# Kernel optimization log

Hardware: AMD Instinct MI355X
Metric: run time of the kernel (lower is better)

The kernel has to match this reference:

```python
import jax, jax.numpy as jnp
import numpy as np

N = 50000
E = 800000
IN_C = 128
HID = 32
HEADS = 4
G = 512      # number of graphs in batch
OUT_C = 100
NEG_SLOPE = 0.2
EPS = 1e-16


def _gat_params(key, f_in, heads, c):
    k1, k2, k3, k4 = jax.random.split(key, 4)
    s = 1.0 / np.sqrt(f_in)
    return {
        'W': jax.random.uniform(k1, (heads * c, f_in), jnp.float32, -s, s),
        'att_src': jax.random.normal(k2, (heads, c), jnp.float32) * 0.1,
        'att_dst': jax.random.normal(k3, (heads, c), jnp.float32) * 0.1,
        'b': jnp.zeros((heads * c,), jnp.float32),
    }


def setup_inputs() -> dict:
    key = jax.random.key(0)
    ks = jax.random.split(key, 8)
    x = jax.random.normal(ks[0], (N, IN_C), jnp.float32)
    edge_index = jax.random.randint(ks[1], (2, E), 0, N, jnp.int64)
    batch = jnp.sort(jax.random.randint(ks[2], (N,), 0, G, jnp.int64))
    p1 = _gat_params(ks[3], IN_C, HEADS, HID)
    p2 = _gat_params(ks[4], HEADS * HID, HEADS, HID)
    p3 = _gat_params(ks[5], HEADS * HID, HEADS, HID)
    s = 1.0 / np.sqrt(HEADS * HID)
    fc_W = jax.random.uniform(ks[6], (OUT_C, HEADS * HID), jnp.float32, -s, s)
    fc_b = jnp.zeros((OUT_C,), jnp.float32)
    return {
        'x': x, 'edge_index': edge_index, 'batch': batch,
        'W1': p1['W'], 'as1': p1['att_src'], 'ad1': p1['att_dst'], 'b1': p1['b'],
        'W2': p2['W'], 'as2': p2['att_src'], 'ad2': p2['att_dst'], 'b2': p2['b'],
        'W3': p3['W'], 'as3': p3['att_src'], 'ad3': p3['att_dst'], 'b3': p3['b'],
        'fc_W': fc_W, 'fc_b': fc_b,
    }


def gat_conv(x, src, dst, W, att_src, att_dst, b):
    # x: [N, F_in] -> h: [N, H, C]
    h = (x @ W.T).reshape(N, HEADS, HID)
    a_src = jnp.einsum('nhc,hc->nh', h, att_src)   # [N, H]
    a_dst = jnp.einsum('nhc,hc->nh', h, att_dst)
    alpha = a_src[src] + a_dst[dst]                 # [E', H]
    alpha = jax.nn.leaky_relu(alpha, NEG_SLOPE)
    # segment softmax over incoming edges of each dst node
    m = jax.ops.segment_max(alpha, dst, num_segments=N)
    alpha = jnp.exp(alpha - m[dst])
    denom = jax.ops.segment_sum(alpha, dst, num_segments=N)
    alpha = alpha / (denom[dst] + EPS)
    msg = alpha[:, :, None] * h[src]                # [E', H, C]
    out = jax.ops.segment_sum(msg, dst, num_segments=N)
    return out.reshape(N, HEADS * HID) + b


def reference(x, edge_index, batch,
              W1, as1, ad1, b1, W2, as2, ad2, b2, W3, as3, ad3, b3,
              fc_W, fc_b):
    # add self loops (PyG GATConv default)
    loops = jnp.arange(N, dtype=edge_index.dtype)
    src = jnp.concatenate([edge_index[0], loops])
    dst = jnp.concatenate([edge_index[1], loops])
    h = jax.nn.elu(gat_conv(x, src, dst, W1, as1, ad1, b1))
    h = jax.nn.elu(gat_conv(h, src, dst, W2, as2, ad2, b2))
    h = jax.nn.elu(gat_conv(h, src, dst, W3, as3, ad3, b3))
    # global mean pool over graphs
    sums = jax.ops.segment_sum(h, batch, num_segments=G)        # [G, H*C]
    cnts = jax.ops.segment_sum(jnp.ones((N,), h.dtype), batch, num_segments=G)
    pooled = sums / jnp.maximum(cnts, 1.0)[:, None]
    # dropout p=0.5 is identity in eval mode
    return pooled @ fc_W.T + fc_b
```

## Files before the change

kernel.cpp:

```cpp
#include <hip/hip_runtime.h>
#include <math.h>

#define NN 50000
#define EE 800000
#define GG 512
#define OUTC 100
#define NEG 0.2f
#define STRIDE 64
#define NPART 8
#define PRNG (NN / NPART)
#define PCHUNK 4096
#define NCHUNK 196
#define SCAT_BLOCKS (NPART * NCHUNK)

#define WROWS 145
#define WCHUNKS 73
#define WLAYER (WCHUNKS * 512)

typedef unsigned int u32;
#define GLOBAL_AS __attribute__((address_space(1)))
#define LDS_AS __attribute__((address_space(3)))

typedef __attribute__((ext_vector_type(8))) short bf16x8;
typedef __attribute__((ext_vector_type(8))) short s16x8;
typedef __attribute__((ext_vector_type(8))) unsigned short us8;
typedef __attribute__((ext_vector_type(4))) float f32x4;

__device__ inline ushort f2bf(float v) {
  unsigned u = __float_as_uint(v);
  unsigned r = (u + 0x7fff + ((u >> 16) & 1)) >> 16;
  return (ushort)r;
}

__global__ __launch_bounds__(256) void k_scatter_prep(const int* __restrict__ ei,
    int* __restrict__ cursor, ushort* __restrict__ srcs,
    const float* __restrict__ W0, const float* __restrict__ W1, const float* __restrict__ W2,
    const float* __restrict__ as0, const float* __restrict__ as1, const float* __restrict__ as2,
    const float* __restrict__ ad0, const float* __restrict__ ad1, const float* __restrict__ ad2,
    ushort* __restrict__ wg) {
  if (blockIdx.x < SCAT_BLOCKS) {
    int part = blockIdx.x & (NPART - 1);
    int chunk = blockIdx.x >> 3;
    int plo = part * PRNG, phi = plo + PRNG;
    int base = chunk * PCHUNK + (threadIdx.x << 2);
    int4 d[4];
    bool lv[4];
#pragma unroll
    for (int it = 0; it < 4; ++it) {
      int e = base + (it << 10);
      lv[it] = (e < EE);
      if (lv[it]) d[it] = *(const int4*)&ei[EE + e];
      else        d[it] = make_int4(-1, -1, -1, -1);
    }
#pragma unroll
    for (int it = 0; it < 4; ++it) {
      if (!lv[it]) continue;
      int e = base + (it << 10);
      int4 dd = d[it];
      bool m0 = (dd.x >= plo) & (dd.x < phi);
      bool m1 = (dd.y >= plo) & (dd.y < phi);
      bool m2 = (dd.z >= plo) & (dd.z < phi);
      bool m3 = (dd.w >= plo) & (dd.w < phi);
      if (m0 | m1 | m2 | m3) {
        int4 s4 = *(const int4*)&ei[e];
        if (m0) { int p = atomicAdd(&cursor[dd.x], 1); if (p < STRIDE) srcs[(dd.x << 6) + p] = (ushort)s4.x; }
        if (m1) { int p = atomicAdd(&cursor[dd.y], 1); if (p < STRIDE) srcs[(dd.y << 6) + p] = (ushort)s4.y; }
        if (m2) { int p = atomicAdd(&cursor[dd.z], 1); if (p < STRIDE) srcs[(dd.z << 6) + p] = (ushort)s4.z; }
        if (m3) { int p = atomicAdd(&cursor[dd.w], 1); if (p < STRIDE) srcs[(dd.w << 6) + p] = (ushort)s4.w; }
      }
    }
  } else {
    int pb = blockIdx.x - SCAT_BLOCKS;
    int layer = pb / 68, bx = pb % 68;
    const float* W  = (layer == 0) ? W0 : (layer == 1) ? W1 : W2;
    const float* av = (layer == 0) ? as0 : (layer == 1) ? as1 : as2;
    const float* dv = (layer == 0) ? ad0 : (layer == 1) ? ad1 : ad2;
    ushort* wgL = wg + (size_t)layer * WLAYER;
    int idx = bx * 256 + threadIdx.x;
    if (bx < 64) {
      int row = idx >> 7, col = idx & 127;
      int c = col >> 3, j = col & 7;
      float v = W[idx];
      ushort hb = f2bf(v);
      float hf = __uint_as_float(((unsigned)hb) << 16);
      wgL[((size_t)c * WROWS + row) * 8 + j] = hb;
      wgL[((size_t)(16 + c) * WROWS + row) * 8 + j] = f2bf(v - hf);
    } else {
      int j2 = idx - 64 * 256;
      int j = j2 >> 7, k = j2 & 127;
      int head = j & 3;
      const float* vec = (j < 4) ? &av[head * 32] : &dv[head * 32];
      float dot = 0.f;
#pragma unroll
      for (int c = 0; c < 32; c++) dot += W[(head * 32 + c) * 128 + k] * vec[c];
      ushort hb = f2bf(dot);
      float hf = __uint_as_float(((unsigned)hb) << 16);
      int c16 = k >> 3, jj = k & 7;
      wgL[((size_t)c16 * WROWS + 128 + j) * 8 + jj] = hb;
      wgL[((size_t)(16 + c16) * WROWS + 128 + j) * 8 + jj] = f2bf(dot - hf);
      wgL[((size_t)c16 * WROWS + 136 + j) * 8 + jj] = 0;
      wgL[((size_t)(16 + c16) * WROWS + 136 + j) * 8 + jj] = 0;
    }
  }
}

__global__ __launch_bounds__(512) void k_gemm_mfma(const float* __restrict__ feat,
    const ushort* __restrict__ wg,
    short* __restrict__ hq, float* __restrict__ asp, float* __restrict__ adstf) {
  __shared__ alignas(16) ushort lds[WLAYER];
  int t = threadIdx.x;
  int wave = t >> 6, lane = t & 63;
  int quad = lane >> 4, r16 = lane & 15;

#pragma unroll
  for (int i = 0; i < 10; ++i) {
    int chunk = i * 8 + wave;
    if (chunk < WCHUNKS) {
      int off = chunk * 512 + lane * 8;
      __builtin_amdgcn_global_load_lds((const GLOBAL_AS u32*)&wg[off],
                                       (LDS_AS u32*)&lds[off], 16, 0, 0);
    }
  }

  int n0 = blockIdx.x * 128;
  int rowA = n0 + wave * 16 + r16;
  bool valid = rowA < NN;
  float4 f[8];
#pragma unroll
  for (int ks = 0; ks < 4; ++ks) {
    if (valid) {
      const float4* fp = (const float4*)&feat[(size_t)rowA * 128 + ks * 32 + quad * 8];
      f[ks * 2] = fp[0];
      f[ks * 2 + 1] = fp[1];
    } else {
      f[ks * 2] = make_float4(0.f, 0.f, 0.f, 0.f);
      f[ks * 2 + 1] = f[ks * 2];
    }
  }
  __syncthreads();

  f32x4 acc[9];
#pragma unroll
  for (int nt = 0; nt < 9; nt++) acc[nt] = (f32x4)0.f;

#pragma unroll
  for (int ks = 0; ks < 4; ks++) {
    bf16x8 ah, al;
    {
      float4 va = f[ks * 2], vb = f[ks * 2 + 1];
      float vv[8] = {va.x, va.y, va.z, va.w, vb.x, vb.y, vb.z, vb.w};
      us8 hh, ll;
#pragma unroll
      for (int j = 0; j < 8; j++) {
        ushort hb = f2bf(vv[j]);
        float hf = __uint_as_float(((unsigned)hb) << 16);
        hh[j] = hb;
        ll[j] = (ushort)(__float_as_uint(vv[j] - hf) >> 16);
      }
      ah = (bf16x8)hh;
      al = (bf16x8)ll;
    }
    int cc = ks * 4 + quad;
#pragma unroll
    for (int nt = 0; nt < 9; nt++) {
      int wrow = (nt < 8) ? (nt * 16 + r16) : (128 + r16);
      bf16x8 bh = *(const bf16x8*)&lds[((size_t)cc * WROWS + wrow) * 8];
      bf16x8 bl = *(const bf16x8*)&lds[((size_t)(16 + cc) * WROWS + wrow) * 8];
      acc[nt] = __builtin_amdgcn_mfma_f32_16x16x32_bf16(ah, bh, acc[nt], 0, 0, 0);
      acc[nt] = __builtin_amdgcn_mfma_f32_16x16x32_bf16(al, bh, acc[nt], 0, 0, 0);
      acc[nt] = __builtin_amdgcn_mfma_f32_16x16x32_bf16(ah, bl, acc[nt], 0, 0, 0);
    }
  }

#pragma unroll
  for (int reg = 0; reg < 4; reg++) {
    float am = 0.f;
#pragma unroll
    for (int nt = 0; nt < 8; nt++) am = fmaxf(am, fabsf(acc[nt][reg]));
#pragma unroll
    for (int off = 1; off < 16; off <<= 1) am = fmaxf(am, __shfl_xor(am, off));
    int node = n0 + wave * 16 + quad * 4 + reg;
    if (node < NN) {
      float amc = fmaxf(am, 1e-20f);
      float rq = 32767.f / amc;
      if (r16 < 4) asp[node * 8 + r16] = acc[8][reg];
      else if (r16 < 8) adstf[node * 4 + r16 - 4] = acc[8][reg];
      else if (r16 == 8) asp[node * 8 + 4] = amc * (1.f / 32767.f);
      short* dq = &hq[(size_t)node * 128 + r16];
#pragma unroll
      for (int nt = 0; nt < 8; nt++)
        dq[nt * 16] = (short)__float2int_rn(acc[nt][reg] * rq);
    }
  }
}

__global__ __launch_bounds__(256) void k_gather(const short* __restrict__ hq,
    const float* __restrict__ asp,
    const float4* __restrict__ adst,
    const int* __restrict__ cursor, const ushort* __restrict__ srcs,
    const float* __restrict__ bias, float* __restrict__ outf) {
  __shared__ alignas(16) int   s_src[2][4][4][16];
  __shared__ alignas(16) float s_wt[2][4][4][4][20];

  int wave = threadIdx.x >> 6, lane = threadIdx.x & 63;
  int grp = lane >> 4;
  int gl = lane & 15;
  int node = blockIdx.x * 16 + wave * 4 + grp;
  int head = gl >> 2;
  int c0 = gl << 3;

  int deg = 0, e0 = 0;
  float4 ad = make_float4(0.f, 0.f, 0.f, 0.f);
  if (node < NN) {
    deg = min(cursor[node], STRIDE);
    e0 = node << 6;
    ad = adst[node];
  }
  int rounds = (deg + 15) >> 4;

  float acc[8];
#pragma unroll
  for (int i = 0; i < 8; i++) acc[i] = 0.f;
  float ws0 = 0.f, ws1 = 0.f, ws2 = 0.f, ws3 = 0.f;
  float wself = 0.f;

  int nsn = 0, nlive = 0;

  auto phase1 = [&](int r) {
    int j = (r << 4) + gl;
    nlive = (j < deg);
    nsn = nlive ? (int)srcs[e0 + j] : 0;
  };

  auto phase2 = [&](int b) {
    float q0 = 0.f, q1 = 0.f, q2 = 0.f, q3 = 0.f;
    if (nlive) {
      const float4 a = *(const float4*)&asp[nsn * 8];
      float sc = asp[nsn * 8 + 4];
      float v, w0, w1, w2, w3;
      v = a.x + ad.x; v = v > 0.f ? v : NEG * v; w0 = __expf(v);
      v = a.y + ad.y; v = v > 0.f ? v : NEG * v; w1 = __expf(v);
      v = a.z + ad.z; v = v > 0.f ? v : NEG * v; w2 = __expf(v);
      v = a.w + ad.w; v = v > 0.f ? v : NEG * v; w3 = __expf(v);
      ws0 += w0; ws1 += w1; ws2 += w2; ws3 += w3;
      q0 = w0 * sc; q1 = w1 * sc; q2 = w2 * sc; q3 = w3 * sc;
    }
    s_src[b][wave][grp][gl] = nsn << 7;
    s_wt[b][wave][grp][0][gl] = q0;
    s_wt[b][wave][grp][1][gl] = q1;
    s_wt[b][wave][grp][2][gl] = q2;
    s_wt[b][wave][grp][3][gl] = q3;
  };

  auto consume = [&](int r, int b) {
    int cnt = deg - (r << 4);
    cnt = min(cnt, 16);
    const int* srow = &s_src[b][wave][grp][0];
    const float* wrow = &s_wt[b][wave][grp][head][0];
#pragma unroll
    for (int c = 0; c < 2; ++c) {
      int k0 = c << 3;
      if (k0 < cnt) {
        int4 sa = *(const int4*)&srow[k0];
        int4 sb = *(const int4*)&srow[k0 + 4];
        float4 wa = *(const float4*)&wrow[k0];
        float4 wb = *(const float4*)&wrow[k0 + 4];
        s16x8 qa = *(const s16x8*)&hq[sa.x + c0];
        s16x8 qb = *(const s16x8*)&hq[sa.y + c0];
        s16x8 qc = *(const s16x8*)&hq[sa.z + c0];
        s16x8 qd = *(const s16x8*)&hq[sa.w + c0];
        s16x8 qe = *(const s16x8*)&hq[sb.x + c0];
        s16x8 qf = *(const s16x8*)&hq[sb.y + c0];
        s16x8 qg = *(const s16x8*)&hq[sb.z + c0];
        s16x8 qh = *(const s16x8*)&hq[sb.w + c0];
#pragma unroll
        for (int i = 0; i < 8; i++) acc[i] = fmaf(wa.x, (float)qa[i], acc[i]);
#pragma unroll
        for (int i = 0; i < 8; i++) acc[i] = fmaf(wa.y, (float)qb[i], acc[i]);
#pragma unroll
        for (int i = 0; i < 8; i++) acc[i] = fmaf(wa.z, (float)qc[i], acc[i]);
#pragma unroll
        for (int i = 0; i < 8; i++) acc[i] = fmaf(wa.w, (float)qd[i], acc[i]);
        if (k0 + 4 < cnt) {
#pragma unroll
          for (int i = 0; i < 8; i++) acc[i] = fmaf(wb.x, (float)qe[i], acc[i]);
#pragma unroll
          for (int i = 0; i < 8; i++) acc[i] = fmaf(wb.y, (float)qf[i], acc[i]);
#pragma unroll
          for (int i = 0; i < 8; i++) acc[i] = fmaf(wb.z, (float)qg[i], acc[i]);
#pragma unroll
          for (int i = 0; i < 8; i++) acc[i] = fmaf(wb.w, (float)qh[i], acc[i]);
        }
      }
    }
  };

  phase1(0);

  if (node < NN) {
    const float4 a = *(const float4*)&asp[node * 8];
    float sc = asp[node * 8 + 4];
    float v, w0, w1, w2, w3;
    v = a.x + ad.x; v = v > 0.f ? v : NEG * v; w0 = __expf(v);
    v = a.y + ad.y; v = v > 0.f ? v : NEG * v; w1 = __expf(v);
    v = a.z + ad.z; v = v > 0.f ? v : NEG * v; w2 = __expf(v);
    v = a.w + ad.w; v = v > 0.f ? v : NEG * v; w3 = __expf(v);
    float wh = (head == 0) ? w0 : (head == 1) ? w1 : (head == 2) ? w2 : w3;
    wself = wh;
    float wssc = wh * sc;
    s16x8 qs = *(const s16x8*)&hq[(node << 7) + c0];
#pragma unroll
    for (int i = 0; i < 8; i++) acc[i] = wssc * (float)qs[i];
  }

  if (rounds > 0) {
    phase2(0);
    for (int r = 0; r < rounds; ++r) {
      int b = r & 1;
      if (r + 1 < rounds) phase1(r + 1);
      consume(r, b);
      if (r + 1 < rounds) phase2(b ^ 1);
    }
  }

#pragma unroll
  for (int off = 1; off < 16; off <<= 1) {
    ws0 += __shfl_xor(ws0, off);
    ws1 += __shfl_xor(ws1, off);
    ws2 += __shfl_xor(ws2, off);
    ws3 += __shfl_xor(ws3, off);
  }

  if (node < NN) {
    float wsum = wself + ((head == 0) ? ws0 : (head == 1) ? ws1 : (head == 2) ? ws2 : ws3);
    float rcp = 1.f / (wsum + 1e-16f);
    float4 bv0 = *(const float4*)&bias[c0];
    float4 bv1 = *(const float4*)&bias[c0 + 4];
    float bb[8] = {bv0.x, bv0.y, bv0.z, bv0.w, bv1.x, bv1.y, bv1.z, bv1.w};
    float o[8];
#pragma unroll
    for (int i = 0; i < 8; i++) {
      float v = acc[i] * rcp + bb[i];
      o[i] = v > 0.f ? v : expm1f(v);
    }
    *(float4*)&outf[(size_t)node * 128 + c0] = make_float4(o[0], o[1], o[2], o[3]);
    *(float4*)&outf[(size_t)node * 128 + c0 + 4] = make_float4(o[4], o[5], o[6], o[7]);
  }
}

__global__ __launch_bounds__(128) void k_pool(const float* __restrict__ feat,
    const int* __restrict__ batch, float* __restrict__ pooled, float* __restrict__ cnt) {
  int n0 = blockIdx.x * 32;
  int c = threadIdx.x;
  float acc = 0.f; int curg = -1;
  for (int i = 0; i < 32; i++) {
    int n = n0 + i;
    if (n >= NN) break;
    int g = batch[n];
    if (g != curg) {
      if (curg >= 0) atomicAdd(&pooled[curg * 128 + c], acc);
      acc = 0.f; curg = g;
    }
    acc += feat[n * 128 + c];
  }
  if (curg >= 0) atomicAdd(&pooled[curg * 128 + c], acc);
  if (threadIdx.x == 0) {
    float cc = 0.f; int cg = -1;
    for (int i = 0; i < 32; i++) {
      int n = n0 + i;
      if (n >= NN) break;
      int g = batch[n];
      if (g != cg) { if (cg >= 0) atomicAdd(&cnt[cg], cc); cc = 0.f; cg = g; }
      cc += 1.f;
    }
    if (cg >= 0) atomicAdd(&cnt[cg], cc);
  }
}

__global__ __launch_bounds__(128) void k_fc(const float* __restrict__ pooled,
    const float* __restrict__ cnt, const float* __restrict__ fcW,
    const float* __restrict__ fcb, float* __restrict__ out) {
  int g = blockIdx.x;
  __shared__ float p[128];
  int t = threadIdx.x;
  float inv = 1.0f / fmaxf(cnt[g], 1.0f);
  p[t] = pooled[g * 128 + t] * inv;
  __syncthreads();
  if (t < OUTC) {
    float acc = fcb[t];
    const float4* wr = (const float4*)&fcW[t * 128];
    const float4* pp = (const float4*)p;
#pragma unroll
    for (int i = 0; i < 32; i++) {
      float4 w = wr[i], pv = pp[i];
      acc = fmaf(w.x, pv.x, fmaf(w.y, pv.y, fmaf(w.z, pv.z, fmaf(w.w, pv.w, acc))));
    }
    out[g * OUTC + t] = acc;
  }
}

extern "C" void kernel_launch(void* const* d_in, const int* in_sizes, int n_in,
                              void* d_out, int out_size, void* d_ws, size_t ws_size,
                              hipStream_t stream) {
  const float* x    = (const float*)d_in[0];
  const int*   ei   = (const int*)d_in[1];
  const int*   batch= (const int*)d_in[2];
  const float* W1   = (const float*)d_in[3];
  const float* as1  = (const float*)d_in[4];
  const float* ad1  = (const float*)d_in[5];
  const float* b1   = (const float*)d_in[6];
  const float* W2   = (const float*)d_in[7];
  const float* as2  = (const float*)d_in[8];
  const float* ad2  = (const float*)d_in[9];
  const float* b2   = (const float*)d_in[10];
  const float* W3   = (const float*)d_in[11];
  const float* as3  = (const float*)d_in[12];
  const float* ad3  = (const float*)d_in[13];
  const float* b3   = (const float*)d_in[14];
  const float* fcW  = (const float*)d_in[15];
  const float* fcb  = (const float*)d_in[16];
  float* out = (float*)d_out;

  char* p = (char*)d_ws;
  auto alloc = [&](size_t bytes) { char* r = p; p += (bytes + 255) & ~(size_t)255; return r; };
  short* hq     = (short*)alloc((size_t)NN * 128 * 2);
  float* asp    = (float*)alloc((size_t)NN * 8 * 4);
  float* buf0   = (float*)alloc((size_t)NN * 128 * 4);
  float* adstv  = (float*)alloc((size_t)NN * 4 * 4);
  char*  zbase  = p;
  int*   cursor = (int*)alloc((size_t)NN * 4);
  float* pooled = (float*)alloc((size_t)GG * 128 * 4);
  float* cnt    = (float*)alloc((size_t)GG * 4);
  size_t zlen   = (size_t)(p - zbase);
  ushort* srcs  = (ushort*)alloc((size_t)NN * STRIDE * 2);
  ushort* wg    = (ushort*)alloc((size_t)3 * WLAYER * 2);

  hipMemsetAsync(zbase, 0, zlen, stream);

  k_scatter_prep<<<SCAT_BLOCKS + 204, 256, 0, stream>>>(ei, cursor, srcs,
      W1, W2, W3, as1, as2, as3, ad1, ad2, ad3, wg);

  const float* bs[3] = {b1, b2, b3};
  const float* fin = x;
  for (int l = 0; l < 3; l++) {
    k_gemm_mfma<<<(NN + 127) / 128, 512, 0, stream>>>(fin,
        wg + (size_t)l * WLAYER, hq, asp, adstv);
    k_gather<<<(NN + 15) / 16, 256, 0, stream>>>(hq, asp,
        (const float4*)adstv, cursor, srcs, bs[l], buf0);
    fin = buf0;
  }
  k_pool<<<(NN + 31) / 32, 128, 0, stream>>>(buf0, batch, pooled, cnt);
  k_fc<<<GG, 128, 0, stream>>>(pooled, cnt, fcW, fcb, out);
}
```

Before: 321.6 us.

## Fuse global mean pooling into last gather and retune edge scatter chunking

The last GAT layer's gather kernel now accumulates its ELU outputs straight into per-graph pooled sums and counts with atomics. When all four nodes in a wave share a graph, it first reduces them across lanes. This removes the separate pool kernel and the final write and read of the full feature buffer. Separately, the edge scatter now uses half-sized chunks with twice as many blocks, loads src and dst unconditionally with nontemporal loads, and uses per-edge predicates. This trades extra src loads for simpler control flow. More atomics on pooled values in non-uniform waves could add contention.

After: 355.4 us. 10.5% more time.

```diff
diff --git a/kernel.cpp b/kernel.cpp
--- a/kernel.cpp
+++ b/kernel.cpp
@@ -9,8 +9,8 @@
 #define STRIDE 64
 #define NPART 8
 #define PRNG (NN / NPART)
-#define PCHUNK 4096
-#define NCHUNK 196
+#define PCHUNK 2048
+#define NCHUNK 391
 #define SCAT_BLOCKS (NPART * NCHUNK)
 
 #define WROWS 145
@@ -25,6 +25,7 @@
 typedef __attribute__((ext_vector_type(8))) short s16x8;
 typedef __attribute__((ext_vector_type(8))) unsigned short us8;
 typedef __attribute__((ext_vector_type(4))) float f32x4;
+typedef __attribute__((ext_vector_type(4))) int i32x4;
 
 __device__ inline ushort f2bf(float v) {
   unsigned u = __float_as_uint(v);
@@ -43,32 +44,28 @@
     int chunk = blockIdx.x >> 3;
     int plo = part * PRNG, phi = plo + PRNG;
     int base = chunk * PCHUNK + (threadIdx.x << 2);
-    int4 d[4];
-    bool lv[4];
-#pragma unroll
-    for (int it = 0; it < 4; ++it) {
-      int e = base + (it << 10);
-      lv[it] = (e < EE);
-      if (lv[it]) d[it] = *(const int4*)&ei[EE + e];
-      else        d[it] = make_int4(-1, -1, -1, -1);
-    }
-#pragma unroll
-    for (int it = 0; it < 4; ++it) {
-      if (!lv[it]) continue;
-      int e = base + (it << 10);
-      int4 dd = d[it];
-      bool m0 = (dd.x >= plo) & (dd.x < phi);
-      bool m1 = (dd.y >= plo) & (dd.y < phi);
-      bool m2 = (dd.z >= plo) & (dd.z < phi);
-      bool m3 = (dd.w >= plo) & (dd.w < phi);
-      if (m0 | m1 | m2 | m3) {
-        int4 s4 = *(const int4*)&ei[e];
-        if (m0) { int p = atomicAdd(&cursor[dd.x], 1); if (p < STRIDE) srcs[(dd.x << 6) + p] = (ushort)s4.x; }
-        if (m1) { int p = atomicAdd(&cursor[dd.y], 1); if (p < STRIDE) srcs[(dd.y << 6) + p] = (ushort)s4.y; }
-        if (m2) { int p = atomicAdd(&cursor[dd.z], 1); if (p < STRIDE) srcs[(dd.z << 6) + p] = (ushort)s4.z; }
-        if (m3) { int p = atomicAdd(&cursor[dd.w], 1); if (p < STRIDE) srcs[(dd.w << 6) + p] = (ushort)s4.w; }
-      }
-    }
+    bool l0 = base < EE, l1 = (base + 1024) < EE;
+    i32x4 d0, d1, s0, s1;
+    if (l0) {
+      d0 = __builtin_nontemporal_load((const i32x4*)&ei[EE + base]);
+      s0 = __builtin_nontemporal_load((const i32x4*)&ei[base]);
+    }
+    if (l1) {
+      d1 = __builtin_nontemporal_load((const i32x4*)&ei[EE + base + 1024]);
+      s1 = __builtin_nontemporal_load((const i32x4*)&ei[base + 1024]);
+    }
+#define SCAT1(DV, SV) do { \
+      if ((DV) >= plo && (DV) < phi) { \
+        int ppos = atomicAdd(&cursor[DV], 1); \
+        if (ppos < STRIDE) srcs[((unsigned)(DV) << 6) + ppos] = (ushort)(SV); \
+      } } while (0)
+    if (l0) {
+      SCAT1(d0.x, s0.x); SCAT1(d0.y, s0.y); SCAT1(d0.z, s0.z); SCAT1(d0.w, s0.w);
+    }
+    if (l1) {
+      SCAT1(d1.x, s1.x); SCAT1(d1.y, s1.y); SCAT1(d1.z, s1.z); SCAT1(d1.w, s1.w);
+    }
+#undef SCAT1
   } else {
     int pb = blockIdx.x - SCAT_BLOCKS;
     int layer = pb / 68, bx = pb % 68;
@@ -194,11 +191,12 @@
   }
 }
 
-__global__ __launch_bounds__(256) void k_gather(const short* __restrict__ hq,
-    const float* __restrict__ asp,
-    const float4* __restrict__ adst,
+template <int FUSE>
+__device__ __forceinline__ void gather_core(const short* __restrict__ hq,
+    const float* __restrict__ asp, const float4* __restrict__ adst,
     const int* __restrict__ cursor, const ushort* __restrict__ srcs,
-    const float* __restrict__ bias, float* __restrict__ outf) {
+    const float* __restrict__ bias, float* __restrict__ outf,
+    const int* __restrict__ batchv, float* __restrict__ pooled, float* __restrict__ cnt) {
   __shared__ alignas(16) int   s_src[2][4][4][16];
   __shared__ alignas(16) float s_wt[2][4][4][4][20];
 
@@ -211,7 +209,8 @@
 
   int deg = 0, e0 = 0;
   float4 ad = make_float4(0.f, 0.f, 0.f, 0.f);
-  if (node < NN) {
+  bool valid = node < NN;
+  if (valid) {
     deg = min(cursor[node], STRIDE);
     e0 = node << 6;
     ad = adst[node];
@@ -253,14 +252,14 @@
   };
 
   auto consume = [&](int r, int b) {
-    int cnt = deg - (r << 4);
-    cnt = min(cnt, 16);
+    int cnt2 = deg - (r << 4);
+    cnt2 = min(cnt2, 16);
     const int* srow = &s_src[b][wave][grp][0];
     const float* wrow = &s_wt[b][wave][grp][head][0];
 #pragma unroll
     for (int c = 0; c < 2; ++c) {
       int k0 = c << 3;
-      if (k0 < cnt) {
+      if (k0 < cnt2) {
         int4 sa = *(const int4*)&srow[k0];
         int4 sb = *(const int4*)&srow[k0 + 4];
         float4 wa = *(const float4*)&wrow[k0];
@@ -281,7 +280,7 @@
         for (int i = 0; i < 8; i++) acc[i] = fmaf(wa.z, (float)qc[i], acc[i]);
 #pragma unroll
         for (int i = 0; i < 8; i++) acc[i] = fmaf(wa.w, (float)qd[i], acc[i]);
-        if (k0 + 4 < cnt) {
+        if (k0 + 4 < cnt2) {
 #pragma unroll
           for (int i = 0; i < 8; i++) acc[i] = fmaf(wb.x, (float)qe[i], acc[i]);
 #pragma unroll
@@ -297,7 +296,7 @@
 
   phase1(0);
 
-  if (node < NN) {
+  if (valid) {
     const float4 a = *(const float4*)&asp[node * 8];
     float sc = asp[node * 8 + 4];
     float v, w0, w1, w2, w3;
@@ -331,50 +330,64 @@
     ws3 += __shfl_xor(ws3, off);
   }
 
-  if (node < NN) {
+  float o[8];
+  if (valid) {
     float wsum = wself + ((head == 0) ? ws0 : (head == 1) ? ws1 : (head == 2) ? ws2 : ws3);
     float rcp = 1.f / (wsum + 1e-16f);
     float4 bv0 = *(const float4*)&bias[c0];
     float4 bv1 = *(const float4*)&bias[c0 + 4];
     float bb[8] = {bv0.x, bv0.y, bv0.z, bv0.w, bv1.x, bv1.y, bv1.z, bv1.w};
-    float o[8];
 #pragma unroll
     for (int i = 0; i < 8; i++) {
       float v = acc[i] * rcp + bb[i];
       o[i] = v > 0.f ? v : expm1f(v);
     }
-    *(float4*)&outf[(size_t)node * 128 + c0] = make_float4(o[0], o[1], o[2], o[3]);
-    *(float4*)&outf[(size_t)node * 128 + c0 + 4] = make_float4(o[4], o[5], o[6], o[7]);
-  }
-}
-
-__global__ __launch_bounds__(128) void k_pool(const float* __restrict__ feat,
-    const int* __restrict__ batch, float* __restrict__ pooled, float* __restrict__ cnt) {
-  int n0 = blockIdx.x * 32;
-  int c = threadIdx.x;
-  float acc = 0.f; int curg = -1;
-  for (int i = 0; i < 32; i++) {
-    int n = n0 + i;
-    if (n >= NN) break;
-    int g = batch[n];
-    if (g != curg) {
-      if (curg >= 0) atomicAdd(&pooled[curg * 128 + c], acc);
-      acc = 0.f; curg = g;
-    }
-    acc += feat[n * 128 + c];
-  }
-  if (curg >= 0) atomicAdd(&pooled[curg * 128 + c], acc);
-  if (threadIdx.x == 0) {
-    float cc = 0.f; int cg = -1;
-    for (int i = 0; i < 32; i++) {
-      int n = n0 + i;
-      if (n >= NN) break;
-      int g = batch[n];
-      if (g != cg) { if (cg >= 0) atomicAdd(&cnt[cg], cc); cc = 0.f; cg = g; }
-      cc += 1.f;
-    }
-    if (cg >= 0) atomicAdd(&cnt[cg], cc);
-  }
+  } else {
+#pragma unroll
+    for (int i = 0; i < 8; i++) o[i] = 0.f;
+  }
+
+  if (!FUSE) {
+    if (valid) {
+      *(float4*)&outf[(size_t)node * 128 + c0] = make_float4(o[0], o[1], o[2], o[3]);
+      *(float4*)&outf[(size_t)node * 128 + c0 + 4] = make_float4(o[4], o[5], o[6], o[7]);
+    }
+  } else {
+    int g = valid ? batchv[node] : -1;
+    int g1 = __shfl_xor(g, 16);
+    int g2 = __shfl_xor(g, 32);
+    int g3 = __shfl_xor(g, 48);
+    bool uni = (g == g1) && (g == g2) && (g == g3) && (g >= 0);
+    if (uni) {
+#pragma unroll
+      for (int i = 0; i < 8; i++) {
+        float s = o[i];
+        s += __shfl_xor(s, 16);
+        s += __shfl_xor(s, 32);
+        if (lane < 16) atomicAdd(&pooled[g * 128 + c0 + i], s);
+      }
+      if (lane == 0) atomicAdd(&cnt[g], 4.f);
+    } else if (valid) {
+#pragma unroll
+      for (int i = 0; i < 8; i++) atomicAdd(&pooled[g * 128 + c0 + i], o[i]);
+      if (gl == 0) atomicAdd(&cnt[g], 1.f);
+    }
+  }
+}
+
+__global__ __launch_bounds__(256) void k_gather(const short* __restrict__ hq,
+    const float* __restrict__ asp, const float4* __restrict__ adst,
+    const int* __restrict__ cursor, const ushort* __restrict__ srcs,
+    const float* __restrict__ bias, float* __restrict__ outf) {
+  gather_core<0>(hq, asp, adst, cursor, srcs, bias, outf, nullptr, nullptr, nullptr);
+}
+
+__global__ __launch_bounds__(256) void k_gather_pool(const short* __restrict__ hq,
+    const float* __restrict__ asp, const float4* __restrict__ adst,
+    const int* __restrict__ cursor, const ushort* __restrict__ srcs,
+    const float* __restrict__ bias,
+    const int* __restrict__ batchv, float* __restrict__ pooled, float* __restrict__ cnt) {
+  gather_core<1>(hq, asp, adst, cursor, srcs, bias, nullptr, batchv, pooled, cnt);
 }
 
 __global__ __launch_bounds__(128) void k_fc(const float* __restrict__ pooled,
@@ -440,15 +453,17 @@
   k_scatter_prep<<<SCAT_BLOCKS + 204, 256, 0, stream>>>(ei, cursor, srcs,
       W1, W2, W3, as1, as2, as3, ad1, ad2, ad3, wg);
 
-  const float* bs[3] = {b1, b2, b3};
-  const float* fin = x;
-  for (int l = 0; l < 3; l++) {
-    k_gemm_mfma<<<(NN + 127) / 128, 512, 0, stream>>>(fin,
-        wg + (size_t)l * WLAYER, hq, asp, adstv);
-    k_gather<<<(NN + 15) / 16, 256, 0, stream>>>(hq, asp,
-        (const float4*)adstv, cursor, srcs, bs[l], buf0);
-    fin = buf0;
-  }
-  k_pool<<<(NN + 31) / 32, 128, 0, stream>>>(buf0, batch, pooled, cnt);
+  k_gemm_mfma<<<(NN + 127) / 128, 512, 0, stream>>>(x, wg, hq, asp, adstv);
+  k_gather<<<(NN + 15) / 16, 256, 0, stream>>>(hq, asp,
+      (const float4*)adstv, cursor, srcs, b1, buf0);
+  k_gemm_mfma<<<(NN + 127) / 128, 512, 0, stream>>>(buf0,
+      wg + (size_t)WLAYER, hq, asp, adstv);
+  k_gather<<<(NN + 15) / 16, 256, 0, stream>>>(hq, asp,
+      (const float4*)adstv, cursor, srcs, b2, buf0);
+  k_gemm_mfma<<<(NN + 127) / 128, 512, 0, stream>>>(buf0,
+      wg + (size_t)2 * WLAYER, hq, asp, adstv);
+  k_gather_pool<<<(NN + 15) / 16, 256, 0, stream>>>(hq, asp,
+      (const float4*)adstv, cursor, srcs, b3, batch, pooled, cnt);
+
   k_fc<<<GG, 128, 0, stream>>>(pooled, cnt, fcW, fcb, out);
 }
```

## Deepen gather prefetch pipeline and restructure scatter with smaller chunks

Applied to the files above, without the earlier changes.

The gather kernel now prefetches source indices two rounds ahead and issues the attention-score loads for the next round before consuming the current one, so the dependent srcs->asp load chain overlaps with the FMA work. The scatter prep halves the edge chunk per block (more blocks), loads source and destination edge vectors unconditionally with nontemporal loads, and drops the per-quad mask prefilter. This trades extra register pressure and unconditional source loads for better latency hiding.

New measurement: 322.5 us. About the same (+0.3%).

```diff
diff --git a/kernel.cpp b/kernel.cpp
--- a/kernel.cpp
+++ b/kernel.cpp
@@ -9,8 +9,8 @@
 #define STRIDE 64
 #define NPART 8
 #define PRNG (NN / NPART)
-#define PCHUNK 4096
-#define NCHUNK 196
+#define PCHUNK 2048
+#define NCHUNK 391
 #define SCAT_BLOCKS (NPART * NCHUNK)
 
 #define WROWS 145
@@ -25,6 +25,7 @@
 typedef __attribute__((ext_vector_type(8))) short s16x8;
 typedef __attribute__((ext_vector_type(8))) unsigned short us8;
 typedef __attribute__((ext_vector_type(4))) float f32x4;
+typedef __attribute__((ext_vector_type(4))) int i32x4;
 
 __device__ inline ushort f2bf(float v) {
   unsigned u = __float_as_uint(v);
@@ -43,32 +44,28 @@
     int chunk = blockIdx.x >> 3;
     int plo = part * PRNG, phi = plo + PRNG;
     int base = chunk * PCHUNK + (threadIdx.x << 2);
-    int4 d[4];
-    bool lv[4];
-#pragma unroll
-    for (int it = 0; it < 4; ++it) {
-      int e = base + (it << 10);
-      lv[it] = (e < EE);
-      if (lv[it]) d[it] = *(const int4*)&ei[EE + e];
-      else        d[it] = make_int4(-1, -1, -1, -1);
-    }
-#pragma unroll
-    for (int it = 0; it < 4; ++it) {
-      if (!lv[it]) continue;
-      int e = base + (it << 10);
-      int4 dd = d[it];
-      bool m0 = (dd.x >= plo) & (dd.x < phi);
-      bool m1 = (dd.y >= plo) & (dd.y < phi);
-      bool m2 = (dd.z >= plo) & (dd.z < phi);
-      bool m3 = (dd.w >= plo) & (dd.w < phi);
-      if (m0 | m1 | m2 | m3) {
-        int4 s4 = *(const int4*)&ei[e];
-        if (m0) { int p = atomicAdd(&cursor[dd.x], 1); if (p < STRIDE) srcs[(dd.x << 6) + p] = (ushort)s4.x; }
-        if (m1) { int p = atomicAdd(&cursor[dd.y], 1); if (p < STRIDE) srcs[(dd.y << 6) + p] = (ushort)s4.y; }
-        if (m2) { int p = atomicAdd(&cursor[dd.z], 1); if (p < STRIDE) srcs[(dd.z << 6) + p] = (ushort)s4.z; }
-        if (m3) { int p = atomicAdd(&cursor[dd.w], 1); if (p < STRIDE) srcs[(dd.w << 6) + p] = (ushort)s4.w; }
-      }
-    }
+    bool l0 = base < EE, l1 = (base + 1024) < EE;
+    i32x4 d0, d1, s0, s1;
+    if (l0) {
+      d0 = __builtin_nontemporal_load((const i32x4*)&ei[EE + base]);
+      s0 = __builtin_nontemporal_load((const i32x4*)&ei[base]);
+    }
+    if (l1) {
+      d1 = __builtin_nontemporal_load((const i32x4*)&ei[EE + base + 1024]);
+      s1 = __builtin_nontemporal_load((const i32x4*)&ei[base + 1024]);
+    }
+#define SCAT1(DV, SV) do { \
+      if ((DV) >= plo && (DV) < phi) { \
+        int ppos = atomicAdd(&cursor[DV], 1); \
+        if (ppos < STRIDE) srcs[((unsigned)(DV) << 6) + ppos] = (ushort)(SV); \
+      } } while (0)
+    if (l0) {
+      SCAT1(d0.x, s0.x); SCAT1(d0.y, s0.y); SCAT1(d0.z, s0.z); SCAT1(d0.w, s0.w);
+    }
+    if (l1) {
+      SCAT1(d1.x, s1.x); SCAT1(d1.y, s1.y); SCAT1(d1.z, s1.z); SCAT1(d1.w, s1.w);
+    }
+#undef SCAT1
   } else {
     int pb = blockIdx.x - SCAT_BLOCKS;
     int layer = pb / 68, bx = pb % 68;
@@ -211,7 +208,8 @@
 
   int deg = 0, e0 = 0;
   float4 ad = make_float4(0.f, 0.f, 0.f, 0.f);
-  if (node < NN) {
+  bool valid = node < NN;
+  if (valid) {
     deg = min(cursor[node], STRIDE);
     e0 = node << 6;
     ad = adst[node];
@@ -224,19 +222,23 @@
   float ws0 = 0.f, ws1 = 0.f, ws2 = 0.f, ws3 = 0.f;
   float wself = 0.f;
 
-  int nsn = 0, nlive = 0;
-
-  auto phase1 = [&](int r) {
+  auto loadSrc = [&](int r, int& sn, int& lv) {
     int j = (r << 4) + gl;
-    nlive = (j < deg);
-    nsn = nlive ? (int)srcs[e0 + j] : 0;
+    lv = (j < deg);
+    sn = lv ? (int)srcs[e0 + j] : 0;
   };
-
-  auto phase2 = [&](int b) {
+  auto loadAsp = [&](int sn, int lv, float4& a, float& sc) {
+    if (lv) {
+      a = *(const float4*)&asp[sn * 8];
+      sc = asp[sn * 8 + 4];
+    } else {
+      a = make_float4(0.f, 0.f, 0.f, 0.f);
+      sc = 0.f;
+    }
+  };
+  auto finishWrite = [&](int b, int sn, int lv, float4 a, float sc) {
     float q0 = 0.f, q1 = 0.f, q2 = 0.f, q3 = 0.f;
-    if (nlive) {
-      const float4 a = *(const float4*)&asp[nsn * 8];
-      float sc = asp[nsn * 8 + 4];
+    if (lv) {
       float v, w0, w1, w2, w3;
       v = a.x + ad.x; v = v > 0.f ? v : NEG * v; w0 = __expf(v);
       v = a.y + ad.y; v = v > 0.f ? v : NEG * v; w1 = __expf(v);
@@ -245,7 +247,7 @@
       ws0 += w0; ws1 += w1; ws2 += w2; ws3 += w3;
       q0 = w0 * sc; q1 = w1 * sc; q2 = w2 * sc; q3 = w3 * sc;
     }
-    s_src[b][wave][grp][gl] = nsn << 7;
+    s_src[b][wave][grp][gl] = sn << 7;
     s_wt[b][wave][grp][0][gl] = q0;
     s_wt[b][wave][grp][1][gl] = q1;
     s_wt[b][wave][grp][2][gl] = q2;
@@ -253,14 +255,14 @@
   };
 
   auto consume = [&](int r, int b) {
-    int cnt = deg - (r << 4);
-    cnt = min(cnt, 16);
+    int cnt2 = deg - (r << 4);
+    cnt2 = min(cnt2, 16);
     const int* srow = &s_src[b][wave][grp][0];
     const float* wrow = &s_wt[b][wave][grp][head][0];
 #pragma unroll
     for (int c = 0; c < 2; ++c) {
       int k0 = c << 3;
-      if (k0 < cnt) {
+      if (k0 < cnt2) {
         int4 sa = *(const int4*)&srow[k0];
         int4 sb = *(const int4*)&srow[k0 + 4];
         float4 wa = *(const float4*)&wrow[k0];
@@ -281,7 +283,7 @@
         for (int i = 0; i < 8; i++) acc[i] = fmaf(wa.z, (float)qc[i], acc[i]);
 #pragma unroll
         for (int i = 0; i < 8; i++) acc[i] = fmaf(wa.w, (float)qd[i], acc[i]);
-        if (k0 + 4 < cnt) {
+        if (k0 + 4 < cnt2) {
 #pragma unroll
           for (int i = 0; i < 8; i++) acc[i] = fmaf(wb.x, (float)qe[i], acc[i]);
 #pragma unroll
@@ -295,9 +297,16 @@
     }
   };
 
-  phase1(0);
-
-  if (node < NN) {
+  int sn0 = 0, lv0 = 0, sn1 = 0, lv1 = 0, sn2 = 0, lv2 = 0;
+  float4 a0; float sc0;
+
+  if (rounds > 0) {
+    loadSrc(0, sn0, lv0);
+    if (rounds > 1) loadSrc(1, sn1, lv1);
+    loadAsp(sn0, lv0, a0, sc0);
+  }
+
+  if (valid) {
     const float4 a = *(const float4*)&asp[node * 8];
     float sc = asp[node * 8 + 4];
     float v, w0, w1, w2, w3;
@@ -314,12 +323,15 @@
   }
 
   if (rounds > 0) {
-    phase2(0);
+    finishWrite(0, sn0, lv0, a0, sc0);
     for (int r = 0; r < rounds; ++r) {
       int b = r & 1;
-      if (r + 1 < rounds) phase1(r + 1);
+      if (r + 2 < rounds) loadSrc(r + 2, sn2, lv2);
+      float4 aX = make_float4(0.f, 0.f, 0.f, 0.f); float scX = 0.f;
+      if (r + 1 < rounds) loadAsp(sn1, lv1, aX, scX);
       consume(r, b);
-      if (r + 1 < rounds) phase2(b ^ 1);
+      if (r + 1 < rounds) finishWrite(b ^ 1, sn1, lv1, aX, scX);
+      sn1 = sn2; lv1 = lv2;
     }
   }
 
@@ -331,7 +343,7 @@
     ws3 += __shfl_xor(ws3, off);
   }
 
-  if (node < NN) {
+  if (valid) {
     float wsum = wself + ((head == 0) ? ws0 : (head == 1) ? ws1 : (head == 2) ? ws2 : ws3);
     float rcp = 1.f / (wsum + 1e-16f);
     float4 bv0 = *(const float4*)&bias[c0];
```
